# Kernel optimization log

Measured on AMD Instinct MI355X. Metric: run time of the kernel, lower is better.

The kernel has to match this reference:

```python
import jax, jax.numpy as jnp
import numpy as np

HS, LEVELS, E = 64, 16, 2
MIN_RES, MAX_RES = 32, 512
MAX_N_DENSE = 256 ** 3
N_ENC = 2 ** 19
MAX_FREQ = 2
PRIMES = np.array([1, 2654435761, 805459861], dtype=np.uint32)
_OFFS = np.stack(np.meshgrid(np.arange(2), np.arange(2), np.arange(2), indexing='ij'), -1).reshape(8, 3).astype(np.int32)


def _level_meta():
    # geometric growth of per-level resolution, dense grid below MAX_N_DENSE else hashed
    growth = np.exp((np.log(MAX_RES) - np.log(MIN_RES)) / (LEVELS - 1))
    metas, off = [], 0
    for l in range(LEVELS):
        res = int(np.floor(MIN_RES * growth ** l))
        dense = (res + 1) ** 3 <= MAX_N_DENSE
        size = (res + 1) ** 3 if dense else N_ENC
        metas.append((res, dense, off))
        off += size
    return metas, off


def _encode(x, table):
    # x: [N,3] in [0,1); table: [total_entries, E] concatenated per-level tables
    metas, _ = _level_meta()
    outs = []
    for res, dense, off in metas:
        xl = x * res
        c0 = jnp.clip(jnp.floor(xl), 0, res - 1).astype(jnp.int32)  # [N,3]
        w = xl - c0.astype(x.dtype)
        corners = c0[:, None, :] + _OFFS  # [N,8,3]
        if dense:
            stride = np.array([1, res + 1, (res + 1) ** 2], dtype=np.int64)
            idx = (corners.astype(jnp.int64) * stride).sum(-1).astype(jnp.int32)
        else:
            cu = corners.astype(jnp.uint32)
            idx = (cu[..., 0] * PRIMES[0]) ^ (cu[..., 1] * PRIMES[1]) ^ (cu[..., 2] * PRIMES[2])
            idx = (idx & np.uint32(N_ENC - 1)).astype(jnp.int32)
        vals = table[off + idx]  # [N,8,E]
        cw = jnp.where(_OFFS[None] == 1, w[:, None, :], 1.0 - w[:, None, :]).prod(-1)  # [N,8]
        outs.append((vals * cw[..., None]).sum(1))
    return jnp.concatenate(outs, -1)  # [N, LEVELS*E]


def setup_inputs() -> dict:
    key = jax.random.key(0)
    ks = jax.random.split(key, 18)
    N = 2_000_000
    _, total = _level_meta()
    def lin(k, i, o):
        return jax.random.normal(k, (i, o), jnp.float32) * (1.0 / np.sqrt(i))
    inp = {
        'coordinates': jax.random.uniform(ks[0], (N, 3), jnp.float32),
        'directions': jax.random.normal(ks[1], (N, 3), jnp.float32),
        'table': jax.random.uniform(ks[2], (total, E), jnp.float32, -1e-4, 1e-4),
        'fw1': lin(ks[3], LEVELS * E, HS), 'fb1': jnp.zeros((HS,), jnp.float32),
        'fw2': lin(ks[4], HS, HS), 'fb2': jnp.zeros((HS,), jnp.float32),
        'fw3': lin(ks[5], HS, 16), 'fb3': jnp.zeros((16,), jnp.float32).at[0].set(-1.0),
        'rw1': lin(ks[6], 16 + 15, HS), 'rb1': jnp.zeros((HS,), jnp.float32),
        'rw2': lin(ks[7], HS, HS), 'rb2': jnp.zeros((HS,), jnp.float32),
        'rw3': lin(ks[8], HS, HS), 'rb3': jnp.zeros((HS,), jnp.float32),
        'rw4': lin(ks[9], HS, 3), 'rb4': jnp.zeros((3,), jnp.float32),
    }
    return inp


def reference(coordinates, directions, table, fw1, fb1, fw2, fb2, fw3, fb3,
              rw1, rb1, rw2, rb2, rw3, rb3, rw4, rb4):
    emb = _encode(coordinates, table)  # [N,32]
    h = jax.nn.relu(emb @ fw1 + fb1)
    h = jax.nn.relu(h @ fw2 + fb2)
    feat = h @ fw3 + fb3  # [N,16]
    sigma = jnp.exp(feat[..., :1])
    freqs = 2.0 ** jnp.arange(MAX_FREQ, dtype=jnp.float32)  # [1,2]
    encs = (directions[..., None] * freqs).reshape(directions.shape[:-1] + (3 * MAX_FREQ,))
    pe = jnp.concatenate([directions, jnp.sin(encs), jnp.cos(encs)], -1)  # [N,15]
    f = jnp.concatenate([feat, pe], -1)  # [N,31]
    h = jax.nn.relu(f @ rw1 + rb1)
    h = jax.nn.relu(h @ rw2 + rb2)
    h = jax.nn.relu(h @ rw3 + rb3)
    rgb = jax.nn.sigmoid(h @ rw4 + rb4)
    return jnp.concatenate([rgb, sigma], -1)  # [N,4]
```

## Files before the change

kernel.cpp:

```cpp
#include <hip/hip_runtime.h>
#include <hip/hip_fp16.h>
#include <math.h>

#define BLK 128
#define EBLK 256
#define NBINS (1 << 18)
#define Q_SCALE 65536.0f
#define Q_DESCALE 0x1p-16f

typedef __attribute__((ext_vector_type(8))) _Float16 half8;
typedef __attribute__((ext_vector_type(4))) float f32x4;
typedef __attribute__((ext_vector_type(2))) float f32x2;

#define FO_L1 0
#define FO_L2 2048
#define FO_L3 6144
#define FO_R1 7168
#define FO_R2 9216
#define FO_R3 13312
#define FO_R4 17408
#define FRAG_TOTAL 18432

__device__ __forceinline__ unsigned mexp(unsigned v) {
    v &= 0x3FF;
    v = (v | (v << 16)) & 0x030000FF;
    v = (v | (v << 8))  & 0x0300F00F;
    v = (v | (v << 4))  & 0x030C30C3;
    v = (v | (v << 2))  & 0x09249249;
    return v;
}
__device__ __forceinline__ unsigned morton_key(float x, float y, float z) {
    int bx = (int)(x * 64.f); bx = bx < 0 ? 0 : (bx > 63 ? 63 : bx);
    int by = (int)(y * 64.f); by = by < 0 ? 0 : (by > 63 ? 63 : by);
    int bz = (int)(z * 64.f); bz = bz < 0 ? 0 : (bz > 63 ? 63 : bz);
    return (mexp((unsigned)bx) << 2) | (mexp((unsigned)by) << 1) | mexp((unsigned)bz);
}

__global__ __launch_bounds__(256) void cvt_table_fp8(const float4* __restrict__ src,
                                                     unsigned* __restrict__ dst, int npair)
{
    int i = blockIdx.x * 256 + threadIdx.x;
    const int stride = gridDim.x * 256;
    for (; i < npair; i += stride) {
        const float4 v = src[i];
        const int lo = __builtin_amdgcn_cvt_pk_fp8_f32(v.x * Q_SCALE, v.y * Q_SCALE, 0, false);
        const int hi = __builtin_amdgcn_cvt_pk_fp8_f32(v.z * Q_SCALE, v.w * Q_SCALE, 0, false);
        dst[i] = ((unsigned)lo & 0xFFFFu) | (((unsigned)hi & 0xFFFFu) << 16);
    }
}

__global__ __launch_bounds__(256) void prep_frags(
    const float* __restrict__ fw1, const float* __restrict__ fw2, const float* __restrict__ fw3,
    const float* __restrict__ rw1, const float* __restrict__ rw2, const float* __restrict__ rw3,
    const float* __restrict__ rw4, _Float16* __restrict__ frag)
{
    const int gid = blockIdx.x * 256 + threadIdx.x;
    if (gid >= FRAG_TOTAL) return;
    constexpr int offs[8] = {FO_L1, FO_L2, FO_L3, FO_R1, FO_R2, FO_R3, FO_R4, FRAG_TOTAL};
    constexpr int Ks[7]   = {32, 64, 64, 31, 64, 64, 64};
    constexpr int NO[7]   = {64, 64, 16, 64, 64, 64, 3};
    constexpr int NKs[7]  = {1, 2, 2, 1, 2, 2, 2};
    int layer = 0;
    #pragma unroll
    for (int i = 1; i < 7; ++i) if (gid >= offs[i]) layer = i;
    const float* W = fw1;
    if (layer == 1) W = fw2; else if (layer == 2) W = fw3;
    else if (layer == 3) W = rw1; else if (layer == 4) W = rw2;
    else if (layer == 5) W = rw3; else if (layer == 6) W = rw4;

    const int e = gid - offs[layer];
    const int nk = NKs[layer];
    const int blk = e >> 9, within = e & 511;
    const int t = blk / nk, ks = blk - t * nk;
    const int lane = within >> 3, i = within & 7;
    const int k = ks * 32 + (lane >> 4) * 8 + i;
    const int col = t * 16 + (lane & 15);
    float v = 0.f;
    if (k < Ks[layer] && col < NO[layer]) v = W[k * NO[layer] + col];
    frag[gid] = (_Float16)v;
}

__global__ __launch_bounds__(256) void hist_build(const float* __restrict__ coords,
                                                  unsigned* __restrict__ hist, int N)
{
    const int i = blockIdx.x * 256 + threadIdx.x;
    if (i >= N) return;
    const unsigned key = morton_key(coords[3*i+0], coords[3*i+1], coords[3*i+2]);
    atomicAdd(&hist[key], 1u);
}

__global__ __launch_bounds__(256) void scan1(unsigned* __restrict__ hist, unsigned* __restrict__ bsum)
{
    __shared__ unsigned sa[256], sb[256];
    const int t = threadIdx.x;
    const unsigned base = blockIdx.x * 1024u + (unsigned)t * 4u;
    const unsigned v0 = hist[base+0], v1 = hist[base+1], v2 = hist[base+2], v3 = hist[base+3];
    const unsigned sum = v0 + v1 + v2 + v3;
    sa[t] = sum; __syncthreads();
    unsigned* src = sa; unsigned* dst = sb;
    for (int off = 1; off < 256; off <<= 1) {
        dst[t] = src[t] + (t >= off ? src[t - off] : 0u);
        __syncthreads();
        unsigned* tmp = src; src = dst; dst = tmp;
    }
    const unsigned incl = src[t];
    unsigned run = incl - sum;
    hist[base+0] = run; run += v0;
    hist[base+1] = run; run += v1;
    hist[base+2] = run; run += v2;
// ... 9 lines not shown
    sa[t] = v; __syncthreads();
    unsigned* src = sa; unsigned* dst = sb;
    for (int off = 1; off < 256; off <<= 1) {
        dst[t] = src[t] + (t >= off ? src[t - off] : 0u);
        __syncthreads();
        unsigned* tmp = src; src = dst; dst = tmp;
    }
    bsum[t] = src[t] - v;
}

__global__ __launch_bounds__(256) void scan3(const unsigned* __restrict__ hist,
                                             const unsigned* __restrict__ bsum,
                                             unsigned* __restrict__ cursor)
{
    const int i = blockIdx.x * 256 + threadIdx.x;
    cursor[i] = hist[i] + bsum[i >> 10];
}

__global__ __launch_bounds__(256) void scatter_pts(const float* __restrict__ coords,
                                                   const float* __restrict__ dirs,
                                                   unsigned* __restrict__ cursor,
                                                   float4* __restrict__ cS,
                                                   float4* __restrict__ dS, int N)
{
    const int i = blockIdx.x * 256 + threadIdx.x;
    if (i >= N) return;
    const float x = coords[3*i+0], y = coords[3*i+1], z = coords[3*i+2];
    const unsigned key = morton_key(x, y, z);
    const unsigned slot = atomicAdd(&cursor[key], 1u);
    cS[slot] = make_float4(x, y, z, __uint_as_float((unsigned)i));
    dS[slot] = make_float4(dirs[3*i+0], dirs[3*i+1], dirs[3*i+2], __uint_as_float((unsigned)i));
}

#define LVL_CONSTS \
    constexpr int RES[16] = {32,38,46,55,67,80,97,116,140,168,203,244,294,353,425,512}; \
    constexpr int DN [16] = {1,1,1,1,1,1,1,1,1,1,1,1,0,0,0,0}; \
    constexpr int OFF[16] = {0,35937,95256,199079,374695,689127,1220568,2161760, \
                             3763373,6566594,11393403,19883067,34589192,35113480, \
                             35637768,36162056}; \
    constexpr unsigned NMASK = (1u << 19) - 1u;

__device__ __forceinline__ void corner_idx(int l, int res, bool dense,
                                           int cx, int cy, int cz, int (&idx)[8])
{
    constexpr unsigned NMASK2 = (1u << 19) - 1u;
    #pragma unroll
    for (int c = 0; c < 8; ++c) {
        const int dx = (c >> 2) & 1, dy = (c >> 1) & 1, dz = c & 1;
        if (dense) {
            idx[c] = (cx + dx) + (cy + dy) * (res + 1) + (cz + dz) * (res + 1) * (res + 1);
        } else {
            const unsigned ux = (unsigned)(cx + dx);
            const unsigned uy = (unsigned)(cy + dy);
            const unsigned uz = (unsigned)(cz + dz);
            const unsigned hh = ux ^ (uy * 2654435761u) ^ (uz * 805459861u);
            idx[c] = (int)(hh & NMASK2);
        }
    }
}

__device__ __forceinline__ void encode_point_q(float x, float y, float z,
                                               const unsigned short* __restrict__ tableQ,
                                               float (&emb)[32])
{
    LVL_CONSTS
    #pragma unroll
    for (int l = 0; l < 16; ++l) {
        const int res = RES[l];
        const float xl = x * (float)res, yl = y * (float)res, zl = z * (float)res;
        int cx = (int)floorf(xl); cx = cx < 0 ? 0 : (cx > res-1 ? res-1 : cx);
        int cy = (int)floorf(yl); cy = cy < 0 ? 0 : (cy > res-1 ? res-1 : cy);
        int cz = (int)floorf(zl); cz = cz < 0 ? 0 : (cz > res-1 ? res-1 : cz);
        const float wx = xl - (float)cx, wy = yl - (float)cy, wz = zl - (float)cz;

        int idx[8];
        corner_idx(l, res, DN[l] != 0, cx, cy, cz, idx);

        unsigned qv[8];
        #pragma unroll
        for (int c = 0; c < 8; ++c) qv[c] = tableQ[OFF[l] + idx[c]];

        float e0 = 0.f, e1 = 0.f;
        #pragma unroll
        for (int c = 0; c < 8; ++c) {
            const int dx = (c >> 2) & 1, dy = (c >> 1) & 1, dz = c & 1;
            const float w = (dx ? wx : 1.f - wx) * (dy ? wy : 1.f - wy) * (dz ? wz : 1.f - wz);
            const f32x2 vf = __builtin_amdgcn_cvt_pk_f32_fp8((int)qv[c], false);
            e0 = fmaf(vf.x, w, e0);
            e1 = fmaf(vf.y, w, e1);
        }
        emb[2*l+0] = e0 * Q_DESCALE;
        emb[2*l+1] = e1 * Q_DESCALE;
    }
}

__device__ __forceinline__ void encode_point_f(float x, float y, float z,
                                               const float* __restrict__ tableF,
                                               float (&emb)[32])
{
    LVL_CONSTS
    #pragma unroll
    for (int l = 0; l < 16; ++l) {
        const int res = RES[l];
        const float xl = x * (float)res, yl = y * (float)res, zl = z * (float)res;
        int cx = (int)floorf(xl); cx = cx < 0 ? 0 : (cx > res-1 ? res-1 : cx);
        int cy = (int)floorf(yl); cy = cy < 0 ? 0 : (cy > res-1 ? res-1 : cy);
        int cz = (int)floorf(zl); cz = cz < 0 ? 0 : (cz > res-1 ? res-1 : cz);
        const float wx = xl - (float)cx, wy = yl - (float)cy, wz = zl - (float)cz;
        int idx[8];
        corner_idx(l, res, DN[l] != 0, cx, cy, cz, idx);
        float e0 = 0.f, e1 = 0.f;
        #pragma unroll
        for (int c = 0; c < 8; ++c) {
            const int dx = (c >> 2) & 1, dy = (c >> 1) & 1, dz = c & 1;
            const float w = (dx ? wx : 1.f - wx) * (dy ? wy : 1.f - wy) * (dz ? wz : 1.f - wz);
            const float2 v = *reinterpret_cast<const float2*>(tableF + (size_t)2 * (size_t)(OFF[l] + idx[c]));
            e0 = fmaf(v.x, w, e0);
            e1 = fmaf(v.y, w, e1);
        }
        emb[2*l+0] = e0;
        emb[2*l+1] = e1;
    }
}

__global__ __launch_bounds__(EBLK, 8) void ngp_encode(
    const float4* __restrict__ cS,
    const unsigned short* __restrict__ tableQ,
    uint4* __restrict__ emb_out, int N)
{
    const unsigned nwg = gridDim.x;
    const unsigned bid = blockIdx.x;
    const unsigned qn = nwg >> 3, rn = nwg & 7;
    const unsigned xc = bid & 7, ib = bid >> 3;
    const unsigned nb = (xc < rn ? xc * (qn + 1) : rn * (qn + 1) + (xc - rn) * qn) + ib;

    const int gi = (int)(nb * EBLK + threadIdx.x);
    if (gi >= N) return;

    const float4 c = cS[gi];
    float emb[32];
    encode_point_q(c.x, c.y, c.z, tableQ, emb);

    unsigned packed[16];
    #pragma unroll
    for (int i = 0; i < 16; ++i) {
        const __half2 h = __floats2half2_rn(emb[2*i+0], emb[2*i+1]);
        packed[i] = *reinterpret_cast<const unsigned*>(&h);
    }
    uint4* dst = emb_out + (size_t)gi * 4;
    #pragma unroll
    for (int k = 0; k < 4; ++k)
        dst[k] = make_uint4(packed[4*k+0], packed[4*k+1], packed[4*k+2], packed[4*k+3]);
}

__device__ __forceinline__ half8 ldfrag(const _Float16* __restrict__ frags, int off, int l) {
    return *reinterpret_cast<const half8*>(frags + off + l * 8);
}
__device__ __forceinline__ int swz(int f, int p) {
    return ((((f >> 3) + p) & 7) << 3) | (f & 7);
}
__device__ __forceinline__ half8 loadA(const _Float16* T, int p, int kb) {
    return *reinterpret_cast<const half8*>(T + p * 64 + ((((kb >> 3) + p) & 7) << 3));
}

template<bool RELU>
__device__ __forceinline__ void storeD4(_Float16* T, const f32x4 (&acc)[4], int p16, int g) {
    #pragma unroll
    for (int t = 0; t < 4; ++t) {
        #pragma unroll
        for (int r = 0; r < 4; ++r) {
            float v = acc[t][r];
            if (RELU) v = fmaxf(v, 0.f);
            const int p = g * 4 + r, f = t * 16 + p16;
            T[p * 64 + swz(f, p)] = (_Float16)v;
        }
    }
}

__global__ __launch_bounds__(256) void ngp_mlp_mfma(
    const _Float16* __restrict__ embws,
    const float4* __restrict__ dS,
    const _Float16* __restrict__ frags,
    const float* __restrict__ fb1, const float* __restrict__ fb2, const float* __restrict__ fb3,
    const float* __restrict__ rb1, const float* __restrict__ rb2, const float* __restrict__ rb3,
    const float* __restrict__ rb4,
    float* __restrict__ out, int N)
{
    __shared__ _Float16 tbuf[4][16 * 64];
    __shared__ float obuf[4][64];
    const int tid = threadIdx.x;
    const int wv = tid >> 6, l = tid & 63;
    const int p16 = l & 15, g = l >> 4;
    const int base = (blockIdx.x * 4 + wv) * 16;
    _Float16* T = tbuf[wv];
    float* O = obuf[wv];

    int pidx = base + p16; if (pidx >= N) pidx = N - 1;
    const float4 d4 = dS[pidx];

    half8 a0 = *reinterpret_cast<const half8*>(embws + (size_t)pidx * 32 + g * 8);
    f32x4 acc[4];
    half8 a1[2];

    __builtin_amdgcn_s_setprio(1);
    #pragma unroll
    for (int t = 0; t < 4; ++t) {
        const float b = fb1[t * 16 + p16];
        f32x4 c = {b, b, b, b};
        acc[t] = __builtin_amdgcn_mfma_f32_16x16x32_f16(a0, ldfrag(frags, FO_L1 + t * 512, l), c, 0, 0, 0);
    }
    __builtin_amdgcn_s_setprio(0);
    storeD4<true>(T, acc, p16, g);
    a1[0] = loadA(T, p16, g * 8); a1[1] = loadA(T, p16, 32 + g * 8);

    __builtin_amdgcn_s_setprio(1);
    #pragma unroll
    for (int t = 0; t < 4; ++t) {
        const float b = fb2[t * 16 + p16];
        f32x4 c = {b, b, b, b};
        c = __builtin_amdgcn_mfma_f32_16x16x32_f16(a1[0], ldfrag(frags, FO_L2 + (t * 2 + 0) * 512, l), c, 0, 0, 0);
        acc[t] = __builtin_amdgcn_mfma_f32_16x16x32_f16(a1[1], ldfrag(frags, FO_L2 + (t * 2 + 1) * 512, l), c, 0, 0, 0);
    }
    __builtin_amdgcn_s_setprio(0);
    storeD4<true>(T, acc, p16, g);
    a1[0] = loadA(T, p16, g * 8); a1[1] = loadA(T, p16, 32 + g * 8);

    {
        const float b = fb3[p16];
        f32x4 c = {b, b, b, b};
        __builtin_amdgcn_s_setprio(1);
        c = __builtin_amdgcn_mfma_f32_16x16x32_f16(a1[0], ldfrag(frags, FO_L3 + 0, l), c, 0, 0, 0);
        c = __builtin_amdgcn_mfma_f32_16x16x32_f16(a1[1], ldfrag(frags, FO_L3 + 512, l), c, 0, 0, 0);
        __builtin_amdgcn_s_setprio(0);
        if (p16 == 0) {
            #pragma unroll
            for (int r = 0; r < 4; ++r) O[(g * 4 + r) * 4 + 3] = __expf(c[r]);
        }
        #pragma unroll
        for (int r = 0; r < 4; ++r) {
            const int p = g * 4 + r, f = p16;
            T[p * 64 + swz(f, p)] = (_Float16)c[r];
        }
    }

    {
        const float dx = d4.x, dy = d4.y, dz = d4.z;
        float pv0, pv1, pv2, pv3;
        if (g == 0)      { pv0 = dx;              pv1 = dy;          pv2 = dz;              pv3 = __sinf(dx); }
        else if (g == 1) { pv0 = __sinf(2.f*dx);  pv1 = __sinf(dy);  pv2 = __sinf(2.f*dy);  pv3 = __sinf(dz); }
        else if (g == 2) { pv0 = __sinf(2.f*dz);  pv1 = __cosf(dx);  pv2 = __cosf(2.f*dx);  pv3 = __cosf(dy); }
        else             { pv0 = __cosf(2.f*dy);  pv1 = __cosf(dz);  pv2 = __cosf(2.f*dz);  pv3 = 0.f; }
        const float pv[4] = {pv0, pv1, pv2, pv3};
        #pragma unroll
        for (int j = 0; j < 4; ++j) {
            const int f = 16 + g * 4 + j;
            T[p16 * 64 + swz(f, p16)] = (_Float16)pv[j];
        }
    }
    half8 ar = loadA(T, p16, g * 8);

    __builtin_amdgcn_s_setprio(1);
    #pragma unroll
    for (int t = 0; t < 4; ++t) {
        const float b = rb1[t * 16 + p16];
        f32x4 c = {b, b, b, b};
        acc[t] = __builtin_amdgcn_mfma_f32_16x16x32_f16(ar, ldfrag(frags, FO_R1 + t * 512, l), c, 0, 0, 0);
    }
    __builtin_amdgcn_s_setprio(0);
    storeD4<true>(T, acc, p16, g);
    a1[0] = loadA(T, p16, g * 8); a1[1] = loadA(T, p16, 32 + g * 8);

    __builtin_amdgcn_s_setprio(1);
    #pragma unroll
    for (int t = 0; t < 4; ++t) {
        const float b = rb2[t * 16 + p16];
        f32x4 c = {b, b, b, b};
        c = __builtin_amdgcn_mfma_f32_16x16x32_f16(a1[0], ldfrag(frags, FO_R2 + (t * 2 + 0) * 512, l), c, 0, 0, 0);
        acc[t] = __builtin_amdgcn_mfma_f32_16x16x32_f16(a1[1], ldfrag(frags, FO_R2 + (t * 2 + 1) * 512, l), c, 0, 0, 0);
    }
    __builtin_amdgcn_s_setprio(0);
    storeD4<true>(T, acc, p16, g);
    a1[0] = loadA(T, p16, g * 8); a1[1] = loadA(T, p16, 32 + g * 8);

    __builtin_amdgcn_s_setprio(1);
    #pragma unroll
    for (int t = 0; t < 4; ++t) {
        const float b = rb3[t * 16 + p16];
        f32x4 c = {b, b, b, b};
        c = __builtin_amdgcn_mfma_f32_16x16x32_f16(a1[0], ldfrag(frags, FO_R3 + (t * 2 + 0) * 512, l), c, 0, 0, 0);
        acc[t] = __builtin_amdgcn_mfma_f32_16x16x32_f16(a1[1], ldfrag(frags, FO_R3 + (t * 2 + 1) * 512, l), c, 0, 0, 0);
    }
    __builtin_amdgcn_s_setprio(0);
    storeD4<true>(T, acc, p16, g);
    a1[0] = loadA(T, p16, g * 8); a1[1] = loadA(T, p16, 32 + g * 8);

    {
        const float b = (p16 < 3) ? rb4[p16] : 0.f;
        f32x4 c = {b, b, b, b};
        __builtin_amdgcn_s_setprio(1);
        c = __builtin_amdgcn_mfma_f32_16x16x32_f16(a1[0], ldfrag(frags, FO_R4 + 0, l), c, 0, 0, 0);
        c = __builtin_amdgcn_mfma_f32_16x16x32_f16(a1[1], ldfrag(frags, FO_R4 + 512, l), c, 0, 0, 0);
        __builtin_amdgcn_s_setprio(0);
        if (p16 < 3) {
            #pragma unroll
            for (int r = 0; r < 4; ++r)
                O[(g * 4 + r) * 4 + p16] = 1.f / (1.f + __expf(-c[r]));
        }
    }

    if (base + p16 < N) {
        const unsigned orig = __float_as_uint(d4.w);
        out[(size_t)orig * 4 + g] = O[p16 * 4 + g];
    }
}

template<int NIN, int NOUT, bool RELU>
__device__ __forceinline__ void dense_l(const float* __restrict__ W, const float* __restrict__ Bias,
                                        const float* __restrict__ col, float (&out)[NOUT])
{
    #pragma unroll
    for (int j = 0; j < NOUT; ++j) out[j] = Bias[j];
    #pragma unroll 4
    for (int i = 0; i < NIN; ++i) {
        const float a = col[i * BLK];
        const float* Wr = W + i * NOUT;
        #pragma unroll
        for (int j = 0; j < NOUT; ++j) out[j] = fmaf(a, Wr[j], out[j]);
    }
    if (RELU) {
        #pragma unroll
        for (int j = 0; j < NOUT; ++j) out[j] = fmaxf(out[j], 0.f);
    }
}

__device__ __forceinline__ float4 mlp_lds(float* col, float dx0, float dy0, float dz0,
    const float* __restrict__ fw1, const float* __restrict__ fb1,
    const float* __restrict__ fw2, const float* __restrict__ fb2,
    const float* __restrict__ fw3, const float* __restrict__ fb3,
    const float* __restrict__ rw1, const float* __restrict__ rb1,
    const float* __restrict__ rw2, const float* __restrict__ rb2,
    const float* __restrict__ rw3, const float* __restrict__ rb3,
    const float* __restrict__ rw4, const float* __restrict__ rb4)
{
    float h[64];
    dense_l<32, 64, true>(fw1, fb1, col, h);
    #pragma unroll
    for (int j = 0; j < 64; ++j) col[j * BLK] = h[j];
    dense_l<64, 64, true>(fw2, fb2, col, h);
    #pragma unroll
    for (int j = 0; j < 64; ++j) col[j * BLK] = h[j];
    float feat16[16];
    dense_l<64, 16, false>(fw3, fb3, col, feat16);
    const float sigma = expf(feat16[0]);
    #pragma unroll
    for (int j = 0; j < 16; ++j) col[j * BLK] = feat16[j];
    col[16 * BLK] = dx0; col[17 * BLK] = dy0; col[18 * BLK] = dz0;
    {
        float s, c;
        sincosf(dx0,     &s, &c); col[19 * BLK] = s; col[25 * BLK] = c;
        sincosf(2.f*dx0, &s, &c); col[20 * BLK] = s; col[26 * BLK] = c;
        sincosf(dy0,     &s, &c); col[21 * BLK] = s; col[27 * BLK] = c;
        sincosf(2.f*dy0, &s, &c); col[22 * BLK] = s; col[28 * BLK] = c;
        sincosf(dz0,     &s, &c); col[23 * BLK] = s; col[29 * BLK] = c;
        sincosf(2.f*dz0, &s, &c); col[24 * BLK] = s; col[30 * BLK] = c;
// ... 44 lines not shown
    float* col = sbuf + tid;
    #pragma unroll
    for (int j = 0; j < 32; ++j) col[j * BLK] = emb[j];

    const float4 ov = mlp_lds(col, dirs[3*gi+0], dirs[3*gi+1], dirs[3*gi+2],
                              fw1, fb1, fw2, fb2, fw3, fb3,
                              rw1, rb1, rw2, rb2, rw3, rb3, rw4, rb4);
    reinterpret_cast<float4*>(out)[gi] = ov;
}

extern "C" void kernel_launch(void* const* d_in, const int* in_sizes, int n_in,
                              void* d_out, int out_size, void* d_ws, size_t ws_size,
                              hipStream_t stream)
{
    const float* coords = (const float*)d_in[0];
    const float* dirs   = (const float*)d_in[1];
    const float* table  = (const float*)d_in[2];
    const float* fw1 = (const float*)d_in[3];
    const float* fb1 = (const float*)d_in[4];
    const float* fw2 = (const float*)d_in[5];
    const float* fb2 = (const float*)d_in[6];
    const float* fw3 = (const float*)d_in[7];
    const float* fb3 = (const float*)d_in[8];
    const float* rw1 = (const float*)d_in[9];
    const float* rb1 = (const float*)d_in[10];
    const float* rw2 = (const float*)d_in[11];
    const float* rb2 = (const float*)d_in[12];
    const float* rw3 = (const float*)d_in[13];
    const float* rb3 = (const float*)d_in[14];
    const float* rw4 = (const float*)d_in[15];
    const float* rb4 = (const float*)d_in[16];

    const int N = in_sizes[0] / 3;
    const int table_floats = in_sizes[2];
    const int entries = table_floats / 2;

    size_t pos = 0;
    auto take = [&](size_t bytes) { size_t p = pos; pos = (pos + bytes + 255) & ~(size_t)255; return p; };
    const size_t o_tableQ = take((size_t)entries * 2);
    const size_t o_emb    = take((size_t)N * 64);
    const size_t o_cS     = take((size_t)N * 16);
    const size_t o_dS     = take((size_t)N * 16);
    const size_t o_hist   = take((size_t)NBINS * 4);
    const size_t o_cursor = take((size_t)NBINS * 4);
    const size_t o_bsum   = take(256 * 4);
    const size_t o_frag   = take((size_t)FRAG_TOTAL * 2);
    const size_t need_full = pos;

    char* ws = (char*)d_ws;

    if (ws_size >= need_full) {
        unsigned short* tableQ = (unsigned short*)(ws + o_tableQ);
        uint4*     embws  = (uint4*)(ws + o_emb);
        float4*    cS     = (float4*)(ws + o_cS);
        float4*    dS     = (float4*)(ws + o_dS);
        unsigned*  hist   = (unsigned*)(ws + o_hist);
        unsigned*  cursor = (unsigned*)(ws + o_cursor);
        unsigned*  bsum   = (unsigned*)(ws + o_bsum);
        _Float16*  frag   = (_Float16*)(ws + o_frag);

        hipLaunchKernelGGL(cvt_table_fp8, dim3(2048), dim3(256), 0, stream,
                           (const float4*)table, (unsigned*)tableQ, table_floats / 4);
        hipLaunchKernelGGL(prep_frags, dim3(FRAG_TOTAL / 256), dim3(256), 0, stream,
                           fw1, fw2, fw3, rw1, rw2, rw3, rw4, frag);
        hipMemsetAsync(hist, 0, (size_t)NBINS * 4, stream);
        hipLaunchKernelGGL(hist_build, dim3((N + 255) / 256), dim3(256), 0, stream,
                           coords, hist, N);
        hipLaunchKernelGGL(scan1, dim3(NBINS / 1024), dim3(256), 0, stream, hist, bsum);
        hipLaunchKernelGGL(scan2, dim3(1), dim3(256), 0, stream, bsum);
        hipLaunchKernelGGL(scan3, dim3(NBINS / 256), dim3(256), 0, stream, hist, bsum, cursor);
        hipLaunchKernelGGL(scatter_pts, dim3((N + 255) / 256), dim3(256), 0, stream,
                           coords, dirs, cursor, cS, dS, N);
        hipLaunchKernelGGL(ngp_encode, dim3((N + EBLK - 1) / EBLK), dim3(EBLK), 0, stream,
                           cS, tableQ, embws, N);
        hipLaunchKernelGGL(ngp_mlp_mfma, dim3((N + 63) / 64), dim3(256), 0, stream,
                           (const _Float16*)embws, dS, frag,
                           fb1, fb2, fb3, rb1, rb2, rb3, rb4,
                           (float*)d_out, N);
    } else {
        hipLaunchKernelGGL(ngp_fused_f32, dim3((N + BLK - 1) / BLK), dim3(BLK), 0, stream,
                           coords, dirs, table,
                           fw1, fb1, fw2, fb2, fw3, fb3,
                           rw1, rb1, rw2, rb2, rw3, rb3, rw4, rb4,
                           (float*)d_out, N);
    }
}
```

Measured before the change: 924.5 us.

## Morton-block the large dense levels and process two tiles per MLP wave

Re-lays the four largest dense-grid levels of the fp8 table into 64^3 Morton-ordered blocks so the 8 corner gathers land in nearby memory. To do this, table conversion is split into three kernels (low dense, hashed, Morton). The MLP kernel now has each wave handle two 16-point tiles, reusing each weight fragment across both. It also permutes output columns so activations go to LDS as packed half2 pairs. The Morton kernel pads the grids up to block multiples, which enlarges the conversion work and the table footprint. All level offsets and sizes are hardcoded to the given configuration.

After: 909.5 us. Within noise of the previous version (-1.6%).

```diff
diff --git a/kernel.cpp b/kernel.cpp
--- a/kernel.cpp
+++ b/kernel.cpp
@@ -21,6 +21,16 @@
 #define FO_R4 17408
 #define FRAG_TOTAL 18432
 
+#define HOFF0 3764224
+#define MOFF0 5861376
+#define MOFF1 12939264
+#define MOFF2 20017152
+#define MOFF3 36794368
+#define TABQ_ENTRIES 53571584
+#define PAIR_LO 1881687
+#define PAIR_H  1048576
+#define MTOT 47710208
+
 __device__ __forceinline__ unsigned mexp(unsigned v) {
     v &= 0x3FF;
     v = (v | (v << 16)) & 0x030000FF;
@@ -29,6 +39,14 @@
     v = (v | (v << 2))  & 0x09249249;
     return v;
 }
+__device__ __forceinline__ unsigned mcomp(unsigned v) {
+    v &= 0x09249249u;
+    v = (v | (v >> 2)) & 0x030C30C3u;
+    v = (v | (v >> 4)) & 0x0300F00Fu;
+    v = (v | (v >> 8)) & 0x030000FFu;
+    v = (v | (v >> 16)) & 0x3FFu;
+    return v;
+}
 __device__ __forceinline__ unsigned morton_key(float x, float y, float z) {
     int bx = (int)(x * 64.f); bx = bx < 0 ? 0 : (bx > 63 ? 63 : bx);
     int by = (int)(y * 64.f); by = by < 0 ? 0 : (by > 63 ? 63 : by);
@@ -36,17 +54,63 @@
     return (mexp((unsigned)bx) << 2) | (mexp((unsigned)by) << 1) | mexp((unsigned)bz);
 }
 
-__global__ __launch_bounds__(256) void cvt_table_fp8(const float4* __restrict__ src,
-                                                     unsigned* __restrict__ dst, int npair)
-{
-    int i = blockIdx.x * 256 + threadIdx.x;
-    const int stride = gridDim.x * 256;
-    for (; i < npair; i += stride) {
-        const float4 v = src[i];
-        const int lo = __builtin_amdgcn_cvt_pk_fp8_f32(v.x * Q_SCALE, v.y * Q_SCALE, 0, false);
-        const int hi = __builtin_amdgcn_cvt_pk_fp8_f32(v.z * Q_SCALE, v.w * Q_SCALE, 0, false);
-        dst[i] = ((unsigned)lo & 0xFFFFu) | (((unsigned)hi & 0xFFFFu) << 16);
-    }
+__device__ __forceinline__ unsigned pk_fp8(float a, float b) {
+    const int lo = __builtin_amdgcn_cvt_pk_fp8_f32(a * Q_SCALE, b * Q_SCALE, 0, false);
+    return (unsigned)lo & 0xFFFFu;
+}
+
+__global__ __launch_bounds__(256) void cvt_lo(const float4* __restrict__ src,
+                                              unsigned* __restrict__ dst)
+{
+    const int i = blockIdx.x * 256 + threadIdx.x;
+    if (i >= PAIR_LO) return;
+    const float4 v = src[i];
+    dst[i] = pk_fp8(v.x, v.y) | (pk_fp8(v.z, v.w) << 16);
+}
+
+__global__ __launch_bounds__(256) void cvt_hash(const float4* __restrict__ src,
+                                                unsigned* __restrict__ dst)
+{
+    const int i = blockIdx.x * 256 + threadIdx.x;
+    if (i >= PAIR_H) return;
+    const float4 v = src[17294596 + i];
+    dst[HOFF0 / 2 + i] = pk_fp8(v.x, v.y) | (pk_fp8(v.z, v.w) << 16);
+}
+
+__global__ __launch_bounds__(256) void cvt_morton(const float* __restrict__ srcF,
+                                                  unsigned short* __restrict__ dstQ)
+{
+    const unsigned e = blockIdx.x * 256 + threadIdx.x;
+    if (e >= MTOT) return;
+    int j, cnt; unsigned base, moff;
+    if (e < 14155776u) {
+        cnt = 3;
+        if (e < 7077888u) { j = 0; base = 0u;        moff = MOFF0; }
+        else              { j = 1; base = 7077888u;  moff = MOFF1; }
+    } else {
+        cnt = 4;
+        if (e < 30932992u){ j = 2; base = 14155776u; moff = MOFF2; }
+        else              { j = 3; base = 30932992u; moff = MOFF3; }
+    }
+    const unsigned within = e - base;
+    const unsigned blk = within >> 18, lo = within & 0x3FFFFu;
+    unsigned bx, by, bz;
+    if (cnt == 3) { bx = blk % 3u; const unsigned t = blk / 3u; by = t % 3u; bz = t / 3u; }
+    else          { bx = blk & 3u; by = (blk >> 2) & 3u; bz = blk >> 4; }
+    const unsigned x = bx * 64u + mcomp(lo);
+    const unsigned y = by * 64u + mcomp(lo >> 1);
+    const unsigned z = bz * 64u + mcomp(lo >> 2);
+
+    constexpr unsigned RES1[4] = {141u, 169u, 204u, 245u};
+    constexpr unsigned SOFF[4] = {3763373u, 6566594u, 11393403u, 19883067u};
+    const unsigned r1 = RES1[j];
+    unsigned q = 0;
+    if (x < r1 && y < r1 && z < r1) {
+        const size_t se = (size_t)SOFF[j] + x + (size_t)y * r1 + (size_t)z * r1 * r1;
+        const float2 v = *reinterpret_cast<const float2*>(srcF + 2 * se);
+        q = pk_fp8(v.x, v.y);
+    }
+    dstQ[(size_t)moff + within] = (unsigned short)q;
 }
 
 __global__ __launch_bounds__(256) void prep_frags(
@@ -74,7 +138,7 @@
     const int t = blk / nk, ks = blk - t * nk;
     const int lane = within >> 3, i = within & 7;
     const int k = ks * 32 + (lane >> 4) * 8 + i;
-    const int col = t * 16 + (lane & 15);
+    const int col = (NO[layer] == 64) ? ((lane & 15) * 4 + t) : (t * 16 + (lane & 15));
     float v = 0.f;
     if (k < Ks[layer] && col < NO[layer]) v = W[k * NO[layer] + col];
     frag[gid] = (_Float16)v;
@@ -150,97 +214,6 @@
     dS[slot] = make_float4(dirs[3*i+0], dirs[3*i+1], dirs[3*i+2], __uint_as_float((unsigned)i));
 }
 
-#define LVL_CONSTS \
-    constexpr int RES[16] = {32,38,46,55,67,80,97,116,140,168,203,244,294,353,425,512}; \
-    constexpr int DN [16] = {1,1,1,1,1,1,1,1,1,1,1,1,0,0,0,0}; \
-    constexpr int OFF[16] = {0,35937,95256,199079,374695,689127,1220568,2161760, \
-                             3763373,6566594,11393403,19883067,34589192,35113480, \
-                             35637768,36162056}; \
-    constexpr unsigned NMASK = (1u << 19) - 1u;
-
-__device__ __forceinline__ void corner_idx(int l, int res, bool dense,
-                                           int cx, int cy, int cz, int (&idx)[8])
-{
-    constexpr unsigned NMASK2 = (1u << 19) - 1u;
-    #pragma unroll
-    for (int c = 0; c < 8; ++c) {
-        const int dx = (c >> 2) & 1, dy = (c >> 1) & 1, dz = c & 1;
-        if (dense) {
-            idx[c] = (cx + dx) + (cy + dy) * (res + 1) + (cz + dz) * (res + 1) * (res + 1);
-        } else {
-            const unsigned ux = (unsigned)(cx + dx);
-            const unsigned uy = (unsigned)(cy + dy);
-            const unsigned uz = (unsigned)(cz + dz);
-            const unsigned hh = ux ^ (uy * 2654435761u) ^ (uz * 805459861u);
-            idx[c] = (int)(hh & NMASK2);
-        }
-    }
-}
-
-__device__ __forceinline__ void encode_point_q(float x, float y, float z,
-                                               const unsigned short* __restrict__ tableQ,
-                                               float (&emb)[32])
-{
-    LVL_CONSTS
-    #pragma unroll
-    for (int l = 0; l < 16; ++l) {
-        const int res = RES[l];
-        const float xl = x * (float)res, yl = y * (float)res, zl = z * (float)res;
-        int cx = (int)floorf(xl); cx = cx < 0 ? 0 : (cx > res-1 ? res-1 : cx);
-        int cy = (int)floorf(yl); cy = cy < 0 ? 0 : (cy > res-1 ? res-1 : cy);
-        int cz = (int)floorf(zl); cz = cz < 0 ? 0 : (cz > res-1 ? res-1 : cz);
-        const float wx = xl - (float)cx, wy = yl - (float)cy, wz = zl - (float)cz;
-
-        int idx[8];
-        corner_idx(l, res, DN[l] != 0, cx, cy, cz, idx);
-
-        unsigned qv[8];
-        #pragma unroll
-        for (int c = 0; c < 8; ++c) qv[c] = tableQ[OFF[l] + idx[c]];
-
-        float e0 = 0.f, e1 = 0.f;
-        #pragma unroll
-        for (int c = 0; c < 8; ++c) {
-            const int dx = (c >> 2) & 1, dy = (c >> 1) & 1, dz = c & 1;
-            const float w = (dx ? wx : 1.f - wx) * (dy ? wy : 1.f - wy) * (dz ? wz : 1.f - wz);
-            const f32x2 vf = __builtin_amdgcn_cvt_pk_f32_fp8((int)qv[c], false);
-            e0 = fmaf(vf.x, w, e0);
-            e1 = fmaf(vf.y, w, e1);
-        }
-        emb[2*l+0] = e0 * Q_DESCALE;
-        emb[2*l+1] = e1 * Q_DESCALE;
-    }
-}
-
-__device__ __forceinline__ void encode_point_f(float x, float y, float z,
-                                               const float* __restrict__ tableF,
-                                               float (&emb)[32])
-{
-    LVL_CONSTS
-    #pragma unroll
-    for (int l = 0; l < 16; ++l) {
-        const int res = RES[l];
-        const float xl = x * (float)res, yl = y * (float)res, zl = z * (float)res;
-        int cx = (int)floorf(xl); cx = cx < 0 ? 0 : (cx > res-1 ? res-1 : cx);
-        int cy = (int)floorf(yl); cy = cy < 0 ? 0 : (cy > res-1 ? res-1 : cy);
-        int cz = (int)floorf(zl); cz = cz < 0 ? 0 : (cz > res-1 ? res-1 : cz);
-        const float wx = xl - (float)cx, wy = yl - (float)cy, wz = zl - (float)cz;
-        int idx[8];
-        corner_idx(l, res, DN[l] != 0, cx, cy, cz, idx);
-        float e0 = 0.f, e1 = 0.f;
-        #pragma unroll
-        for (int c = 0; c < 8; ++c) {
-            const int dx = (c >> 2) & 1, dy = (c >> 1) & 1, dz = c & 1;
-            const float w = (dx ? wx : 1.f - wx) * (dy ? wy : 1.f - wy) * (dz ? wz : 1.f - wz);
-            const float2 v = *reinterpret_cast<const float2*>(tableF + (size_t)2 * (size_t)(OFF[l] + idx[c]));
-            e0 = fmaf(v.x, w, e0);
-            e1 = fmaf(v.y, w, e1);
-        }
-        emb[2*l+0] = e0;
-        emb[2*l+1] = e1;
-    }
-}
-
 __global__ __launch_bounds__(EBLK, 8) void ngp_encode(
     const float4* __restrict__ cS,
     const unsigned short* __restrict__ tableQ,
@@ -255,9 +228,114 @@
     const int gi = (int)(nb * EBLK + threadIdx.x);
     if (gi >= N) return;
 
-    const float4 c = cS[gi];
+    const float4 cp = cS[gi];
+    const float x = cp.x, y = cp.y, z = cp.z;
+
     float emb[32];
-    encode_point_q(c.x, c.y, c.z, tableQ, emb);
+
+    {
+        constexpr int RES[8] = {32,38,46,55,67,80,97,116};
+        constexpr int OFF[8] = {0,35937,95256,199079,374695,689127,1220568,2161760};
+        #pragma unroll
+        for (int l = 0; l < 8; ++l) {
+            const int res = RES[l];
+            const float xl = x * (float)res, yl = y * (float)res, zl = z * (float)res;
+            int cx = (int)floorf(xl); cx = cx < 0 ? 0 : (cx > res-1 ? res-1 : cx);
+            int cy = (int)floorf(yl); cy = cy < 0 ? 0 : (cy > res-1 ? res-1 : cy);
+            int cz = (int)floorf(zl); cz = cz < 0 ? 0 : (cz > res-1 ? res-1 : cz);
+            const float wx = xl - (float)cx, wy = yl - (float)cy, wz = zl - (float)cz;
+            unsigned qv[8];
+            #pragma unroll
+            for (int c = 0; c < 8; ++c) {
+                const int dx = (c >> 2) & 1, dy = (c >> 1) & 1, dz = c & 1;
+                const int idx = (cx+dx) + (cy+dy)*(res+1) + (cz+dz)*(res+1)*(res+1);
+                qv[c] = tableQ[OFF[l] + idx];
+            }
+            float e0 = 0.f, e1 = 0.f;
+            #pragma unroll
+            for (int c = 0; c < 8; ++c) {
+                const int dx = (c >> 2) & 1, dy = (c >> 1) & 1, dz = c & 1;
+                const float w = (dx ? wx : 1.f-wx)*(dy ? wy : 1.f-wy)*(dz ? wz : 1.f-wz);
+                const f32x2 vf = __builtin_amdgcn_cvt_pk_f32_fp8((int)qv[c], false);
+                e0 = fmaf(vf.x, w, e0); e1 = fmaf(vf.y, w, e1);
+            }
+            emb[2*l+0] = e0 * Q_DESCALE; emb[2*l+1] = e1 * Q_DESCALE;
+        }
+    }
+
+    {
+        constexpr int RESM[4] = {140,168,203,244};
+        constexpr int CNTM[4] = {3,3,4,4};
+        constexpr unsigned MOFF[4] = {MOFF0, MOFF1, MOFF2, MOFF3};
+        #pragma unroll
+        for (int j = 0; j < 4; ++j) {
+            const int res = RESM[j];
+            const int cnt = CNTM[j];
+            const float xl = x * (float)res, yl = y * (float)res, zl = z * (float)res;
+            int cx = (int)floorf(xl); cx = cx < 0 ? 0 : (cx > res-1 ? res-1 : cx);
+            int cy = (int)floorf(yl); cy = cy < 0 ? 0 : (cy > res-1 ? res-1 : cy);
+            int cz = (int)floorf(zl); cz = cz < 0 ? 0 : (cz > res-1 ? res-1 : cz);
+            const float wx = xl - (float)cx, wy = yl - (float)cy, wz = zl - (float)cz;
+
+            const int bx0 = cx >> 6, bx1 = (cx+1) >> 6;
+            const int by0 = cy >> 6, by1 = (cy+1) >> 6;
+            const int bz0 = cz >> 6, bz1 = (cz+1) >> 6;
+            const unsigned mx0 = mexp(cx & 63),     mx1 = mexp((cx+1) & 63);
+            const unsigned my0 = mexp(cy & 63) << 1, my1 = mexp((cy+1) & 63) << 1;
+            const unsigned mz0 = mexp(cz & 63) << 2, mz1 = mexp((cz+1) & 63) << 2;
+
+            unsigned qv[8];
+            #pragma unroll
+            for (int c = 0; c < 8; ++c) {
+                const int dx = (c >> 2) & 1, dy = (c >> 1) & 1, dz = c & 1;
+                const int bx = dx ? bx1 : bx0, by = dy ? by1 : by0, bz = dz ? bz1 : bz0;
+                const unsigned mm = (dx ? mx1 : mx0) | (dy ? my1 : my0) | (dz ? mz1 : mz0);
+                const unsigned blk = (unsigned)((bz * cnt + by) * cnt + bx);
+                qv[c] = tableQ[(size_t)MOFF[j] + ((blk << 18) | mm)];
+            }
+            float e0 = 0.f, e1 = 0.f;
+            #pragma unroll
+            for (int c = 0; c < 8; ++c) {
+                const int dx = (c >> 2) & 1, dy = (c >> 1) & 1, dz = c & 1;
+                const float w = (dx ? wx : 1.f-wx)*(dy ? wy : 1.f-wy)*(dz ? wz : 1.f-wz);
+                const f32x2 vf = __builtin_amdgcn_cvt_pk_f32_fp8((int)qv[c], false);
+                e0 = fmaf(vf.x, w, e0); e1 = fmaf(vf.y, w, e1);
+            }
+            emb[16+2*j+0] = e0 * Q_DESCALE; emb[16+2*j+1] = e1 * Q_DESCALE;
+        }
+    }
+
+    {
+        constexpr int RESH[4] = {294,353,425,512};
+        constexpr unsigned HOFF[4] = {HOFF0, HOFF0+524288, HOFF0+1048576, HOFF0+1572864};
+        constexpr unsigned NMASK = (1u << 19) - 1u;
+        #pragma unroll
+        for (int j = 0; j < 4; ++j) {
+            const int res = RESH[j];
+            const float xl = x * (float)res, yl = y * (float)res, zl = z * (float)res;
+            int cx = (int)floorf(xl); cx = cx < 0 ? 0 : (cx > res-1 ? res-1 : cx);
+            int cy = (int)floorf(yl); cy = cy < 0 ? 0 : (cy > res-1 ? res-1 : cy);
+            int cz = (int)floorf(zl); cz = cz < 0 ? 0 : (cz > res-1 ? res-1 : cz);
+            const float wx = xl - (float)cx, wy = yl - (float)cy, wz = zl - (float)cz;
+            unsigned qv[8];
+            #pragma unroll
+            for (int c = 0; c < 8; ++c) {
+                const int dx = (c >> 2) & 1, dy = (c >> 1) & 1, dz = c & 1;
+                const unsigned hh = (unsigned)(cx+dx) ^ ((unsigned)(cy+dy) * 2654435761u)
+                                  ^ ((unsigned)(cz+dz) * 805459861u);
+                qv[c] = tableQ[HOFF[j] + (hh & NMASK)];
+            }
+            float e0 = 0.f, e1 = 0.f;
+            #pragma unroll
+            for (int c = 0; c < 8; ++c) {
+                const int dx = (c >> 2) & 1, dy = (c >> 1) & 1, dz = c & 1;
+                const float w = (dx ? wx : 1.f-wx)*(dy ? wy : 1.f-wy)*(dz ? wz : 1.f-wz);
+                const f32x2 vf = __builtin_amdgcn_cvt_pk_f32_fp8((int)qv[c], false);
+                e0 = fmaf(vf.x, w, e0); e1 = fmaf(vf.y, w, e1);
+            }
+            emb[24+2*j+0] = e0 * Q_DESCALE; emb[24+2*j+1] = e1 * Q_DESCALE;
+        }
+    }
 
     unsigned packed[16];
     #pragma unroll
@@ -280,20 +358,35 @@
 __device__ __forceinline__ half8 loadA(const _Float16* T, int p, int kb) {
     return *reinterpret_cast<const half8*>(T + p * 64 + ((((kb >> 3) + p) & 7) << 3));
 }
-
 template<bool RELU>
-__device__ __forceinline__ void storeD4(_Float16* T, const f32x4 (&acc)[4], int p16, int g) {
-    #pragma unroll
-    for (int t = 0; t < 4; ++t) {
-        #pragma unroll
-        for (int r = 0; r < 4; ++r) {
-            float v = acc[t][r];
-            if (RELU) v = fmaxf(v, 0.f);
-            const int p = g * 4 + r, f = t * 16 + p16;
-            T[p * 64 + swz(f, p)] = (_Float16)v;
-        }
-    }
-}
+__device__ __forceinline__ void storePair(_Float16* T, const f32x4 (&acc)[4], int p16, int g) {
+    #pragma unroll
+    for (int r = 0; r < 4; ++r) {
+        const int p = g * 4 + r;
+        float v0 = acc[0][r], v1 = acc[1][r], v2 = acc[2][r], v3 = acc[3][r];
+        if (RELU) { v0 = fmaxf(v0,0.f); v1 = fmaxf(v1,0.f); v2 = fmaxf(v2,0.f); v3 = fmaxf(v3,0.f); }
+        const __half2 h01 = __floats2half2_rn(v0, v1);
+        const __half2 h23 = __floats2half2_rn(v2, v3);
+        const int blkb = ((p16 >> 1) + p) & 7;
+        uint2* dst = reinterpret_cast<uint2*>(T + p * 64 + blkb * 8 + 4 * (p16 & 1));
+        *dst = make_uint2(*reinterpret_cast<const unsigned*>(&h01),
+                          *reinterpret_cast<const unsigned*>(&h23));
+    }
+}
+__device__ __forceinline__ void pe_fill(_Float16* T, int p16, int g, float dx, float dy, float dz) {
+    float pv0, pv1, pv2, pv3;
+    if (g == 0)      { pv0 = dx;             pv1 = dy;         pv2 = dz;             pv3 = __sinf(dx); }
+    else if (g == 1) { pv0 = __sinf(2.f*dx); pv1 = __sinf(dy); pv2 = __sinf(2.f*dy); pv3 = __sinf(dz); }
+    else if (g == 2) { pv0 = __sinf(2.f*dz); pv1 = __cosf(dx); pv2 = __cosf(2.f*dx); pv3 = __cosf(dy); }
+    else             { pv0 = __cosf(2.f*dy); pv1 = __cosf(dz); pv2 = __cosf(2.f*dz); pv3 = 0.f; }
+    const float pv[4] = {pv0, pv1, pv2, pv3};
+    #pragma unroll
+    for (int j2 = 0; j2 < 4; ++j2) {
+        const int f = 16 + g * 4 + j2;
+        T[p16 * 64 + swz(f, p16)] = (_Float16)pv[j2];
+    }
+}
+#define MFMA16(a, b, c) __builtin_amdgcn_mfma_f32_16x16x32_f16((a), (b), (c), 0, 0, 0)
 
 __global__ __launch_bounds__(256) void ngp_mlp_mfma(
     const _Float16* __restrict__ embws,
@@ -304,131 +397,161 @@
     const float* __restrict__ rb4,
     float* __restrict__ out, int N)
 {
-    __shared__ _Float16 tbuf[4][16 * 64];
-    __shared__ float obuf[4][64];
+    __shared__ _Float16 tbuf[4][2][16 * 64];
+    __shared__ float obuf[4][2][64];
     const int tid = threadIdx.x;
     const int wv = tid >> 6, l = tid & 63;
     const int p16 = l & 15, g = l >> 4;
-    const int base = (blockIdx.x * 4 + wv) * 16;
-    _Float16* T = tbuf[wv];
-    float* O = obuf[wv];
-
-    int pidx = base + p16; if (pidx >= N) pidx = N - 1;
-    const float4 d4 = dS[pidx];
-
-    half8 a0 = *reinterpret_cast<const half8*>(embws + (size_t)pidx * 32 + g * 8);
-    f32x4 acc[4];
-    half8 a1[2];
+    const int wbase = (blockIdx.x * 4 + wv) * 32;
+    _Float16* T0 = tbuf[wv][0];
+    _Float16* T1 = tbuf[wv][1];
+    float* O0 = obuf[wv][0];
+    float* O1 = obuf[wv][1];
+
+    int pi0 = wbase + p16;      if (pi0 >= N) pi0 = N - 1;
+    int pi1 = wbase + 16 + p16; if (pi1 >= N) pi1 = N - 1;
+    const float4 d0 = dS[pi0];
+    const float4 d1 = dS[pi1];
+
+    f32x4 ac0[4], ac1[4];
+    half8 x00, x01, x10, x11;
+
+    {
+        const half8 a0 = *reinterpret_cast<const half8*>(embws + (size_t)pi0 * 32 + g * 8);
+        const half8 a1 = *reinterpret_cast<const half8*>(embws + (size_t)pi1 * 32 + g * 8);
+        __builtin_amdgcn_s_setprio(1);
+        #pragma unroll
+        for (int t = 0; t < 4; ++t) {
+            const float b = fb1[(p16 << 2) + t];
+            const half8 w = ldfrag(frags, FO_L1 + t * 512, l);
+            f32x4 c = {b, b, b, b};
+            ac0[t] = MFMA16(a0, w, c);
+            ac1[t] = MFMA16(a1, w, c);
+        }
+        __builtin_amdgcn_s_setprio(0);
+    }
+    storePair<true>(T0, ac0, p16, g);
+    storePair<true>(T1, ac1, p16, g);
+    x00 = loadA(T0, p16, g*8); x01 = loadA(T0, p16, 32 + g*8);
+    x10 = loadA(T1, p16, g*8); x11 = loadA(T1, p16, 32 + g*8);
 
     __builtin_amdgcn_s_setprio(1);
     #pragma unroll
     for (int t = 0; t < 4; ++t) {
-        const float b = fb1[t * 16 + p16];
-        f32x4 c = {b, b, b, b};
-        acc[t] = __builtin_amdgcn_mfma_f32_16x16x32_f16(a0, ldfrag(frags, FO_L1 + t * 512, l), c, 0, 0, 0);
+        const float b = fb2[(p16 << 2) + t];
+        const half8 w0 = ldfrag(frags, FO_L2 + (2*t+0) * 512, l);
+        const half8 w1 = ldfrag(frags, FO_L2 + (2*t+1) * 512, l);
+        f32x4 c0 = {b, b, b, b}, c1 = {b, b, b, b};
+        c0 = MFMA16(x00, w0, c0); ac0[t] = MFMA16(x01, w1, c0);
+        c1 = MFMA16(x10, w0, c1); ac1[t] = MFMA16(x11, w1, c1);
     }
     __builtin_amdgcn_s_setprio(0);
-    storeD4<true>(T, acc, p16, g);
-    a1[0] = loadA(T, p16, g * 8); a1[1] = loadA(T, p16, 32 + g * 8);
-
-    __builtin_amdgcn_s_setprio(1);
-    #pragma unroll
-    for (int t = 0; t < 4; ++t) {
-        const float b = fb2[t * 16 + p16];
-        f32x4 c = {b, b, b, b};
-        c = __builtin_amdgcn_mfma_f32_16x16x32_f16(a1[0], ldfrag(frags, FO_L2 + (t * 2 + 0) * 512, l), c, 0, 0, 0);
-        acc[t] = __builtin_amdgcn_mfma_f32_16x16x32_f16(a1[1], ldfrag(frags, FO_L2 + (t * 2 + 1) * 512, l), c, 0, 0, 0);
-    }
-    __builtin_amdgcn_s_setprio(0);
-    storeD4<true>(T, acc, p16, g);
-    a1[0] = loadA(T, p16, g * 8); a1[1] = loadA(T, p16, 32 + g * 8);
+    storePair<true>(T0, ac0, p16, g);
+    storePair<true>(T1, ac1, p16, g);
+    x00 = loadA(T0, p16, g*8); x01 = loadA(T0, p16, 32 + g*8);
+    x10 = loadA(T1, p16, g*8); x11 = loadA(T1, p16, 32 + g*8);
 
     {
         const float b = fb3[p16];
-        f32x4 c = {b, b, b, b};
+        const half8 wa = ldfrag(frags, FO_L3 + 0, l);
+        const half8 wb = ldfrag(frags, FO_L3 + 512, l);
+        f32x4 c0 = {b, b, b, b}, c1 = {b, b, b, b};
         __builtin_amdgcn_s_setprio(1);
-        c = __builtin_amdgcn_mfma_f32_16x16x32_f16(a1[0], ldfrag(frags, FO_L3 + 0, l), c, 0, 0, 0);
-        c = __builtin_amdgcn_mfma_f32_16x16x32_f16(a1[1], ldfrag(frags, FO_L3 + 512, l), c, 0, 0, 0);
+        c0 = MFMA16(x00, wa, c0); c0 = MFMA16(x01, wb, c0);
+        c1 = MFMA16(x10, wa, c1); c1 = MFMA16(x11, wb, c1);
         __builtin_amdgcn_s_setprio(0);
         if (p16 == 0) {
             #pragma unroll
-            for (int r = 0; r < 4; ++r) O[(g * 4 + r) * 4 + 3] = __expf(c[r]);
+            for (int r = 0; r < 4; ++r) {
+                O0[(g*4+r)*4 + 3] = __expf(c0[r]);
+                O1[(g*4+r)*4 + 3] = __expf(c1[r]);
+            }
         }
         #pragma unroll
         for (int r = 0; r < 4; ++r) {
-            const int p = g * 4 + r, f = p16;
-            T[p * 64 + swz(f, p)] = (_Float16)c[r];
+            const int p = g*4 + r;
+            T0[p*64 + swz(p16, p)] = (_Float16)c0[r];
+            T1[p*64 + swz(p16, p)] = (_Float16)c1[r];
         }
     }
 
-    {
-        const float dx = d4.x, dy = d4.y, dz = d4.z;
-        float pv0, pv1, pv2, pv3;
-        if (g == 0)      { pv0 = dx;              pv1 = dy;          pv2 = dz;              pv3 = __sinf(dx); }
-        else if (g == 1) { pv0 = __sinf(2.f*dx);  pv1 = __sinf(dy);  pv2 = __sinf(2.f*dy);  pv3 = __sinf(dz); }
-        else if (g == 2) { pv0 = __sinf(2.f*dz);  pv1 = __cosf(dx);  pv2 = __cosf(2.f*dx);  pv3 = __cosf(dy); }
-        else             { pv0 = __cosf(2.f*dy);  pv1 = __cosf(dz);  pv2 = __cosf(2.f*dz);  pv3 = 0.f; }
-        const float pv[4] = {pv0, pv1, pv2, pv3};
-        #pragma unroll
-        for (int j = 0; j < 4; ++j) {
-            const int f = 16 + g * 4 + j;
-            T[p16 * 64 + swz(f, p16)] = (_Float16)pv[j];
-        }
-    }
-    half8 ar = loadA(T, p16, g * 8);
+    pe_fill(T0, p16, g, d0.x, d0.y, d0.z);
+    pe_fill(T1, p16, g, d1.x, d1.y, d1.z);
+    const half8 ar0 = loadA(T0, p16, g*8);
+    const half8 ar1 = loadA(T1, p16, g*8);
 
     __builtin_amdgcn_s_setprio(1);
     #pragma unroll
     for (int t = 0; t < 4; ++t) {
-        const float b = rb1[t * 16 + p16];
+        const float b = rb1[(p16 << 2) + t];
+        const half8 w = ldfrag(frags, FO_R1 + t * 512, l);
         f32x4 c = {b, b, b, b};
-        acc[t] = __builtin_amdgcn_mfma_f32_16x16x32_f16(ar, ldfrag(frags, FO_R1 + t * 512, l), c, 0, 0, 0);
+        ac0[t] = MFMA16(ar0, w, c);
+        ac1[t] = MFMA16(ar1, w, c);
     }
     __builtin_amdgcn_s_setprio(0);
-    storeD4<true>(T, acc, p16, g);
-    a1[0] = loadA(T, p16, g * 8); a1[1] = loadA(T, p16, 32 + g * 8);
+    storePair<true>(T0, ac0, p16, g);
+    storePair<true>(T1, ac1, p16, g);
+    x00 = loadA(T0, p16, g*8); x01 = loadA(T0, p16, 32 + g*8);
+    x10 = loadA(T1, p16, g*8); x11 = loadA(T1, p16, 32 + g*8);
 
     __builtin_amdgcn_s_setprio(1);
     #pragma unroll
     for (int t = 0; t < 4; ++t) {
-        const float b = rb2[t * 16 + p16];
-        f32x4 c = {b, b, b, b};
-        c = __builtin_amdgcn_mfma_f32_16x16x32_f16(a1[0], ldfrag(frags, FO_R2 + (t * 2 + 0) * 512, l), c, 0, 0, 0);
-        acc[t] = __builtin_amdgcn_mfma_f32_16x16x32_f16(a1[1], ldfrag(frags, FO_R2 + (t * 2 + 1) * 512, l), c, 0, 0, 0);
+        const float b = rb2[(p16 << 2) + t];
+        const half8 w0 = ldfrag(frags, FO_R2 + (2*t+0) * 512, l);
+        const half8 w1 = ldfrag(frags, FO_R2 + (2*t+1) * 512, l);
+        f32x4 c0 = {b, b, b, b}, c1 = {b, b, b, b};
+        c0 = MFMA16(x00, w0, c0); ac0[t] = MFMA16(x01, w1, c0);
+        c1 = MFMA16(x10, w0, c1); ac1[t] = MFMA16(x11, w1, c1);
     }
     __builtin_amdgcn_s_setprio(0);
-    storeD4<true>(T, acc, p16, g);
-    a1[0] = loadA(T, p16, g * 8); a1[1] = loadA(T, p16, 32 + g * 8);
+    storePair<true>(T0, ac0, p16, g);
+    storePair<true>(T1, ac1, p16, g);
+    x00 = loadA(T0, p16, g*8); x01 = loadA(T0, p16, 32 + g*8);
+    x10 = loadA(T1, p16, g*8); x11 = loadA(T1, p16, 32 + g*8);
 
     __builtin_amdgcn_s_setprio(1);
     #pragma unroll
     for (int t = 0; t < 4; ++t) {
-        const float b = rb3[t * 16 + p16];
-        f32x4 c = {b, b, b, b};
-        c = __builtin_amdgcn_mfma_f32_16x16x32_f16(a1[0], ldfrag(frags, FO_R3 + (t * 2 + 0) * 512, l), c, 0, 0, 0);
-        acc[t] = __builtin_amdgcn_mfma_f32_16x16x32_f16(a1[1], ldfrag(frags, FO_R3 + (t * 2 + 1) * 512, l), c, 0, 0, 0);
+        const float b = rb3[(p16 << 2) + t];
+        const half8 w0 = ldfrag(frags, FO_R3 + (2*t+0) * 512, l);
+        const half8 w1 = ldfrag(frags, FO_R3 + (2*t+1) * 512, l);
+        f32x4 c0 = {b, b, b, b}, c1 = {b, b, b, b};
+        c0 = MFMA16(x00, w0, c0); ac0[t] = MFMA16(x01, w1, c0);
+        c1 = MFMA16(x10, w0, c1); ac1[t] = MFMA16(x11, w1, c1);
     }
     __builtin_amdgcn_s_setprio(0);
-    storeD4<true>(T, acc, p16, g);
-    a1[0] = loadA(T, p16, g * 8); a1[1] = loadA(T, p16, 32 + g * 8);
+    storePair<true>(T0, ac0, p16, g);
+    storePair<true>(T1, ac1, p16, g);
+    x00 = loadA(T0, p16, g*8); x01 = loadA(T0, p16, 32 + g*8);
+    x10 = loadA(T1, p16, g*8); x11 = loadA(T1, p16, 32 + g*8);
 
     {
         const float b = (p16 < 3) ? rb4[p16] : 0.f;
-        f32x4 c = {b, b, b, b};
+        const half8 wa = ldfrag(frags, FO_R4 + 0, l);
+        const half8 wb = ldfrag(frags, FO_R4 + 512, l);
+        f32x4 c0 = {b, b, b, b}, c1 = {b, b, b, b};
         __builtin_amdgcn_s_setprio(1);
-        c = __builtin_amdgcn_mfma_f32_16x16x32_f16(a1[0], ldfrag(frags, FO_R4 + 0, l), c, 0, 0, 0);
-        c = __builtin_amdgcn_mfma_f32_16x16x32_f16(a1[1], ldfrag(frags, FO_R4 + 512, l), c, 0, 0, 0);
+        c0 = MFMA16(x00, wa, c0); c0 = MFMA16(x01, wb, c0);
+        c1 = MFMA16(x10, wa, c1); c1 = MFMA16(x11, wb, c1);
         __builtin_amdgcn_s_setprio(0);
         if (p16 < 3) {
             #pragma unroll
-            for (int r = 0; r < 4; ++r)
-                O[(g * 4 + r) * 4 + p16] = 1.f / (1.f + __expf(-c[r]));
+            for (int r = 0; r < 4; ++r) {
+                O0[(g*4+r)*4 + p16] = 1.f / (1.f + __expf(-c0[r]));
+                O1[(g*4+r)*4 + p16] = 1.f / (1.f + __expf(-c1[r]));
+            }
         }
     }
 
-    if (base + p16 < N) {
-        const unsigned orig = __float_as_uint(d4.w);
-        out[(size_t)orig * 4 + g] = O[p16 * 4 + g];
+    if (wbase + p16 < N) {
+        const unsigned orig = __float_as_uint(d0.w);
+        out[(size_t)orig * 4 + g] = O0[p16 * 4 + g];
+    }
+    if (wbase + 16 + p16 < N) {
+        const unsigned orig = __float_as_uint(d1.w);
+        out[(size_t)orig * 4 + g] = O1[p16 * 4 + g];
     }
 }
 
@@ -448,6 +571,44 @@
     if (RELU) {
         #pragma unroll
         for (int j = 0; j < NOUT; ++j) out[j] = fmaxf(out[j], 0.f);
+    }
+}
+
+__device__ __forceinline__ void encode_point_f(float x, float y, float z,
+                                               const float* __restrict__ tableF,
+                                               float (&emb)[32])
+{
+    constexpr int RES[16] = {32,38,46,55,67,80,97,116,140,168,203,244,294,353,425,512};
+    constexpr int DN [16] = {1,1,1,1,1,1,1,1,1,1,1,1,0,0,0,0};
+    constexpr int OFF[16] = {0,35937,95256,199079,374695,689127,1220568,2161760,
+                             3763373,6566594,11393403,19883067,34589192,35113480,
+                             35637768,36162056};
+    constexpr unsigned NMASK = (1u << 19) - 1u;
+    #pragma unroll
+    for (int l = 0; l < 16; ++l) {
+        const int res = RES[l];
+        const float xl = x * (float)res, yl = y * (float)res, zl = z * (float)res;
+        int cx = (int)floorf(xl); cx = cx < 0 ? 0 : (cx > res-1 ? res-1 : cx);
+        int cy = (int)floorf(yl); cy = cy < 0 ? 0 : (cy > res-1 ? res-1 : cy);
+        int cz = (int)floorf(zl); cz = cz < 0 ? 0 : (cz > res-1 ? res-1 : cz);
+        const float wx = xl - (float)cx, wy = yl - (float)cy, wz = zl - (float)cz;
+        float e0 = 0.f, e1 = 0.f;
+        #pragma unroll
+        for (int c = 0; c < 8; ++c) {
+            const int dx = (c >> 2) & 1, dy = (c >> 1) & 1, dz = c & 1;
+            int idx;
+            if (DN[l]) {
+                idx = (cx+dx) + (cy+dy)*(res+1) + (cz+dz)*(res+1)*(res+1);
+            } else {
+                const unsigned hh = (unsigned)(cx+dx) ^ ((unsigned)(cy+dy)*2654435761u)
+                                  ^ ((unsigned)(cz+dz)*805459861u);
+                idx = (int)(hh & NMASK);
+            }
+            const float w = (dx ? wx : 1.f-wx)*(dy ? wy : 1.f-wy)*(dz ? wz : 1.f-wz);
+            const float2 v = *reinterpret_cast<const float2*>(tableF + (size_t)2*(size_t)(OFF[l]+idx));
+            e0 = fmaf(v.x, w, e0); e1 = fmaf(v.y, w, e1);
+        }
+        emb[2*l+0] = e0; emb[2*l+1] = e1;
     }
 }
 
@@ -558,12 +719,10 @@
     const float* rb4 = (const float*)d_in[16];
 
     const int N = in_sizes[0] / 3;
-    const int table_floats = in_sizes[2];
-    const int entries = table_floats / 2;
 
     size_t pos = 0;
     auto take = [&](size_t bytes) { size_t p = pos; pos = (pos + bytes + 255) & ~(size_t)255; return p; };
-    const size_t o_tableQ = take((size_t)entries * 2);
+    const size_t o_tableQ = take((size_t)TABQ_ENTRIES * 2);
     const size_t o_emb    = take((size_t)N * 64);
     const size_t o_cS     = take((size_t)N * 16);
     const size_t o_dS     = take((size_t)N * 16);
@@ -585,8 +744,12 @@
         unsigned*  bsum   = (unsigned*)(ws + o_bsum);
         _Float16*  frag   = (_Float16*)(ws + o_frag);
 
-        hipLaunchKernelGGL(cvt_table_fp8, dim3(2048), dim3(256), 0, stream,
-                           (const float4*)table, (unsigned*)tableQ, table_floats / 4);
+        hipLaunchKernelGGL(cvt_lo, dim3((PAIR_LO + 255) / 256), dim3(256), 0, stream,
+                           (const float4*)table, (unsigned*)tableQ);
+        hipLaunchKernelGGL(cvt_hash, dim3(PAIR_H / 256), dim3(256), 0, stream,
+                           (const float4*)table, (unsigned*)tableQ);
+        hipLaunchKernelGGL(cvt_morton, dim3(MTOT / 256), dim3(256), 0, stream,
+                           table, tableQ);
         hipLaunchKernelGGL(prep_frags, dim3(FRAG_TOTAL / 256), dim3(256), 0, stream,
                            fw1, fw2, fw3, rw1, rw2, rw3, rw4, frag);
         hipMemsetAsync(hist, 0, (size_t)NBINS * 4, stream);
@@ -599,7 +762,7 @@
                            coords, dirs, cursor, cS, dS, N);
         hipLaunchKernelGGL(ngp_encode, dim3((N + EBLK - 1) / EBLK), dim3(EBLK), 0, stream,
                            cS, tableQ, embws, N);
-        hipLaunchKernelGGL(ngp_mlp_mfma, dim3((N + 63) / 64), dim3(256), 0, stream,
+        hipLaunchKernelGGL(ngp_mlp_mfma, dim3((N + 127) / 128), dim3(256), 0, stream,
                            (const _Float16*)embws, dS, frag,
                            fb1, fb2, fb3, rb1, rb2, rb3, rb4,
                            (float*)d_out, N);
```
